# Kernel tuning notes

Hardware: AMD Instinct MI355X
Metric: run time of the kernel (lower is better)

The kernel has to match this reference:

```python
import jax, jax.numpy as jnp
import numpy as np

Z, Y, X = 16, 128, 128
B = 2
N_R, N_L = 12000, 20000   # active voxels per batch element (radar / lidar)
C = 64
IN_DIM = 4
NUM_LAYER = 2
K_LIST = (64, 32)         # knn fan-out = 64 / 2**layer
EPS = 1e-5


def _make_voxels(rng, n_per_batch):
    # unique voxel coords per batch, sorted by linear index (batch-major rows)
    out = []
    for b in range(B):
        lin = np.sort(rng.choice(Z * Y * X, size=n_per_batch, replace=False))
        z = lin // (Y * X); y = (lin // X) % Y; x = lin % X
        out.append(np.stack([np.full(n_per_batch, b), z, y, x], 1))
    return np.concatenate(out, 0).astype(np.int32)


def _nbr_map(coords):
    # 3x3x3 submanifold-conv rulebook: row index of each neighbor, -1 if absent
    b = coords[:, 0].astype(np.int64); z = coords[:, 1]; y = coords[:, 2]; x = coords[:, 3]
    keys = ((b * Z + z) * Y + y) * X + x  # globally sorted
    N = coords.shape[0]
    nbr = np.full((N, 27), -1, np.int64)
    k = 0
    for dz in (-1, 0, 1):
        for dy in (-1, 0, 1):
            for dx in (-1, 0, 1):
                nz, ny, nx = z + dz, y + dy, x + dx
                ok = (nz >= 0) & (nz < Z) & (ny >= 0) & (ny < Y) & (nx >= 0) & (nx < X)
                cand = ((b * Z + nz) * Y + ny) * X + nx
                pos = np.searchsorted(keys, cand)
                pos_c = np.clip(pos, 0, N - 1)
                hit = ok & (keys[pos_c] == cand)
                nbr[:, k] = np.where(hit, pos_c, -1)
                k += 1
    return nbr


def setup_inputs() -> dict:
    rng = np.random.default_rng(0)
    key = jax.random.key(0)
    ks = jax.random.split(key, 16)
    coordsR = _make_voxels(rng, N_R)
    coordsL = _make_voxels(rng, N_L)
    nbrR = _nbr_map(coordsR)
    nbrL = _nbr_map(coordsL)
    NLt = B * N_L
    # knn indices (global row ids into radar rows of same batch)
    knn0 = coordsL[:, 0:1].astype(np.int64) * N_R + rng.integers(0, N_R, (NLt, K_LIST[0]))
    knn1 = coordsL[:, 0:1].astype(np.int64) * N_R + rng.integers(0, N_R, (NLt, K_LIST[1]))
    sc = 1.0 / np.sqrt(27 * C).astype(np.float32)
    inp = {
        "featR": jax.random.normal(ks[0], (B * N_R, IN_DIM), jnp.float32),
        "featL": jax.random.normal(ks[1], (NLt, IN_DIM), jnp.float32),
        "img": jax.random.normal(ks[2], (B, 512), jnp.float32),
        "Win": jax.random.normal(ks[3], (2, IN_DIM, C), jnp.float32) * 0.1,
        "bin_": jnp.zeros((2, C), jnp.float32),
        # [layer, branch(R/L), conv(sp,subm_a,subm_b), 27, Cin, Cout]
        "Wconv": jax.random.normal(ks[4], (NUM_LAYER, 2, 3, 27, C, C), jnp.float32) * sc,
        "bconv": jnp.zeros((NUM_LAYER, 2, 3, C), jnp.float32),
        "bng": jnp.ones((NUM_LAYER, 2, 3, C), jnp.float32),
        "bnb": jnp.zeros((NUM_LAYER, 2, 3, C), jnp.float32),
        "Wimg": jax.random.normal(ks[5], (NUM_LAYER, 512, C), jnp.float32) * 0.05,
        "bimg": jnp.zeros((NUM_LAYER, C), jnp.float32),
        "Wval": jax.random.normal(ks[6], (NUM_LAYER, C, C), jnp.float32) * 0.125,
        "bval": jnp.zeros((NUM_LAYER, C), jnp.float32),
        "Wgate": jax.random.normal(ks[7], (NUM_LAYER, 2 * C, C), jnp.float32) * 0.09,
        "bgate": jnp.zeros((NUM_LAYER, C), jnp.float32),
        "Wbev": jax.random.normal(ks[8], (NUM_LAYER, 2, C * Z, C, 3, 3), jnp.float32) * (1.0 / np.sqrt(C * Z * 9).astype(np.float32)),
        "bbev": jnp.zeros((NUM_LAYER, 2, C), jnp.float32),
        "bntg": jnp.ones((NUM_LAYER, 2, C), jnp.float32),
        "bntb": jnp.zeros((NUM_LAYER, 2, C), jnp.float32),
        "nbrR": jnp.asarray(nbrR),
        "nbrL": jnp.asarray(nbrL),
        "knn0": jnp.asarray(knn0),
        "knn1": jnp.asarray(knn1),
        "coordsR": jnp.asarray(coordsR),
        "coordsL": jnp.asarray(coordsL),
    }
    return inp


def _bn1d(f, g, b):
    m = f.mean(0)
    v = f.var(0)
    return (f - m) / jnp.sqrt(v + EPS) * g + b


def _sconv(f, nbr, W, bias):
    # gather-scatter sparse 3D conv: out[n] = sum_k W[k] @ f[nbr[n,k]]
    mask = (nbr >= 0)[..., None].astype(f.dtype)
    g = f[jnp.clip(nbr, 0)] * mask                 # [N, 27, C]
    return jnp.einsum('nkc,kcd->nd', g, W) + bias


def _branch_block(f, nbr, Wc, bc, g, bt):
    # spconv -> bn -> relu, subm_a -> bn -> relu, subm_b -> bn -> relu
    for j in range(3):
        f = jax.nn.relu(_bn1d(_sconv(f, nbr, Wc[j], bc[j]), g[j], bt[j]))
    return f


def _to_bev(f, coords, Wt, bt, gg, gb):
    dense = jnp.zeros((B, Z, Y, X, C), f.dtype).at[
        coords[:, 0], coords[:, 1], coords[:, 2], coords[:, 3]].add(f)
    x2 = dense.transpose(0, 4, 1, 2, 3).reshape(B, C * Z, Y, X)  # 'b c z y x -> b (c z) y x'
    # ConvTranspose2d(k=3, s=1, p=1) == conv with swapped-IO, spatially flipped kernel, pad 1
    Wk = jnp.transpose(Wt, (1, 0, 2, 3))[:, :, ::-1, ::-1]
    out = jax.lax.conv_general_dilated(x2, Wk, (1, 1), ((1, 1), (1, 1)),
                                       dimension_numbers=('NCHW', 'OIHW', 'NCHW'))
    out = out + bt[:, None, None]
    m = out.mean((0, 2, 3), keepdims=True)
    v = out.var((0, 2, 3), keepdims=True)
    out = (out - m) / jnp.sqrt(v + EPS) * gg[:, None, None] + gb[:, None, None]
    return jax.nn.relu(out)


def reference(featR, featL, img, Win, bin_, Wconv, bconv, bng, bnb, Wimg, bimg,
              Wval, bval, Wgate, bgate, Wbev, bbev, bntg, bntb,
              nbrR, nbrL, knn0, knn1, coordsR, coordsL):
    fR = featR @ Win[0] + bin_[0]   # input_convR (1x1x1)
    fL = featL @ Win[1] + bin_[1]   # input_convL (1x1x1)
    knns = (knn0, knn1)
    bidL = coordsL[:, 0]
    bevs = []
    for l in range(NUM_LAYER):
        fR = _branch_block(fR, nbrR, Wconv[l, 0], bconv[l, 0], bng[l, 0], bnb[l, 0])
        fL = _branch_block(fL, nbrL, Wconv[l, 1], bconv[l, 1], bng[l, 1], bnb[l, 1])
        # knn cross-attention fusion: lidar queries K nearest radar voxels
        key = fR[knns[l]]                                        # [NL, K, C]
        val = jnp.einsum('nkc,cd->nkd', key, Wval[l]) + bval[l]
        attn = jax.nn.softmax(jnp.einsum('nc,nkc->nk', fL, key), axis=-1)
        fused = jnp.einsum('nk,nkd->nd', attn, val)
        imgf = jax.nn.sigmoid(img @ Wimg[l] + bimg[l])           # [B, C] weather condition
        fused = fused * imgf[bidL]
        gate = jax.nn.sigmoid(jnp.concatenate([fL, fused], -1) @ Wgate[l] + bgate[l])
        fL = fL + gate * fused
        bevs.append(_to_bev(fR, coordsR, Wbev[l, 0], bbev[l, 0], bntg[l, 0], bntb[l, 0]))
        bevs.append(_to_bev(fL, coordsL, Wbev[l, 1], bbev[l, 1], bntg[l, 1], bntb[l, 1]))
    return jnp.concatenate(bevs, axis=1)  # [B, 4*C, Y, X]
```

## Files before the change

kernel.cpp:

```cpp
#include <hip/hip_runtime.h>
#include <math.h>

#define NRT 24000
#define NLT 40000

static __device__ __forceinline__ float sigmoidf_(float x){ return 1.0f/(1.0f+expf(-x)); }

static __device__ __forceinline__ int xcd_swz(int bid, int nwg){
  int q = nwg>>3, r = nwg&7, x = bid&7, i = bid>>3;
  return (x<r ? x*(q+1) : r*(q+1)+(x-r)*q) + i;
}

__global__ void k_proj(const float* __restrict__ feat, const float* __restrict__ W,
                       const float* __restrict__ bias, float* __restrict__ out, int N){
  int i = blockIdx.x*256 + threadIdx.x;
  if (i >= N*64) return;
  int n = i >> 6, c = i & 63;
  const float* f = feat + n*4;
  out[i] = fmaf(f[0], W[c], fmaf(f[1], W[64+c], fmaf(f[2], W[128+c], fmaf(f[3], W[192+c], bias[c]))));
}

__global__ void k_mask(const int* __restrict__ nbr, int N, int* __restrict__ mask){
  int n = blockIdx.x*256+threadIdx.x;
  if (n>=N) return;
  const int* row = nbr + (size_t)n*27;
  int m=0;
  #pragma unroll
  for (int k=0;k<27;k++) if (row[k]>=0) m |= 1<<k;
  mask[n]=m;
}

__global__ void k_wsum(const int* __restrict__ mask, int N, int* __restrict__ wsum){
  int n = blockIdx.x*256+threadIdx.x;
  int pc = (n<N)? __popc(mask[n]) : 0;
  #pragma unroll
  for (int s=32;s;s>>=1) pc += __shfl_down(pc, s, 64);
  if ((threadIdx.x&63)==0) wsum[(blockIdx.x*256+threadIdx.x)>>6] = pc;
}

__global__ void k_scan(const int* __restrict__ in, int M, int* __restrict__ out){
  __shared__ int buf[704];
  for (int i=threadIdx.x;i<M;i+=256) buf[i]=in[i];
  __syncthreads();
  if (threadIdx.x==0){ int s=0; for (int i=0;i<M;i++){ int v=buf[i]; buf[i]=s; s+=v; } buf[M]=s; }
  __syncthreads();
  for (int i=threadIdx.x;i<=M;i+=256) out[i]=buf[i];
}

__global__ void k_noff(const int* __restrict__ mask, const int* __restrict__ woff,
                       int N, int* __restrict__ noff){
  int n = blockIdx.x*256+threadIdx.x;
  if (n>=N) return;
  int lane = threadIdx.x&63;
  int pc = __popc(mask[n]);
  int pre = pc;
  #pragma unroll
  for (int s=1;s<64;s<<=1){ int v=__shfl_up(pre, s, 64); if (lane>=s) pre+=v; }
  noff[n] = woff[n>>6] + pre - pc;
  if (n==N-1) noff[N] = woff[N>>6];
}

__global__ void k_kcnt2(const int* __restrict__ mask, int N, int* __restrict__ cnt2){
  int k = blockIdx.x>>3, seg = blockIdx.x&7;
  int s0 = seg*(N/8), s1 = s0 + N/8;
  int c=0;
  for (int n=s0+threadIdx.x;n<s1;n+=256) c += (mask[n]>>k)&1;
  __shared__ int ls[256];
  ls[threadIdx.x]=c; __syncthreads();
  for (int m=128;m;m>>=1){ if (threadIdx.x<m) ls[threadIdx.x]+=ls[threadIdx.x+m]; __syncthreads(); }
  if (threadIdx.x==0) cnt2[blockIdx.x]=ls[0];
}

__global__ void k_kfill2(const int* __restrict__ mask, int N, const int* __restrict__ off2,
                         unsigned* __restrict__ pairs){
  int w = (blockIdx.x*256+threadIdx.x)>>6;
  int lane = threadIdx.x&63;
  int k = w>>3, seg = w&7;
  int s0 = seg*(N/8), s1 = s0 + N/8;
  int base = off2[w];
  for (int n0=s0;n0<s1;n0+=64){
    int n = n0+lane;
    int v = (n<s1) && ((mask[n]>>k)&1);
    unsigned long long bal = __ballot(v);
    if (v) pairs[base + (int)__popcll(bal & ((1ull<<lane)-1))] = ((unsigned)k<<16)|(unsigned)n;
    base += (int)__popcll(bal);
  }
}

__global__ void k_wc(const float* __restrict__ Wconv, float* __restrict__ WcT){
  int i = blockIdx.x*256+threadIdx.x;
  if (i >= 12*27*16*64*4) return;
  int j = i & 3; int r = i >> 2;
  int d = r & 63; r >>= 6;
  int c4 = r & 15; r >>= 4;
  int k = r % 27; int lc = r / 27;
  WcT[i] = Wconv[(size_t)lc*110592 + (size_t)k*4096 + (size_t)(4*c4+j)*64 + d];
}

__global__ void k_spmm(const float* __restrict__ fin, const int* __restrict__ nbr,
                       const int* __restrict__ mask, const int* __restrict__ noff,
                       const int* __restrict__ off2, const unsigned* __restrict__ pairs,
                       const float* __restrict__ W, float* __restrict__ contrib, int nwaves){
  int wid = (blockIdx.x*256+threadIdx.x)>>6;
  int t = threadIdx.x&63;
  int total = off2[216];
  int a = (int)(((long long)wid*total)/nwaves);
  int b = (int)(((long long)(wid+1)*total)/nwaves);
  int kcur = -1;
  float4 wreg[16];
  for (int i=a;i<b;i++){
    unsigned pk = pairs[i];
    int k = pk>>16, n = pk&0xFFFF;
    if (k!=kcur){
      kcur=k;
      const float4* w4 = reinterpret_cast<const float4*>(W) + k*1024 + t;
      #pragma unroll
      for (int c4=0;c4<16;c4++) wreg[c4]=w4[c4*64];
    }
    int nb = nbr[(size_t)n*27+k];
    const float4* fr = reinterpret_cast<const float4*>(fin + (size_t)nb*64);
    float4 a4 = make_float4(0.f,0.f,0.f,0.f);
    #pragma unroll
    for (int c4=0;c4<16;c4++){
      float4 fv = fr[c4];
      a4.x = fmaf(fv.x, wreg[c4].x, a4.x);
      a4.y = fmaf(fv.y, wreg[c4].y, a4.y);
      a4.z = fmaf(fv.z, wreg[c4].z, a4.z);
      a4.w = fmaf(fv.w, wreg[c4].w, a4.w);
    }
    int rank = __popc(mask[n] & ((1<<k)-1));
    contrib[((size_t)noff[n]+rank)*64 + t] = (a4.x+a4.y)+(a4.z+a4.w);
  }
}

__global__ void k_sred(const float* __restrict__ contrib, const int* __restrict__ noff,
                       float* __restrict__ out, int N){
  int n = (blockIdx.x*256+threadIdx.x)>>6;
  if (n>=N) return;
  int t = threadIdx.x&63;
  int j0=noff[n], j1=noff[n+1];
  float s=0.f;
  for (int j=j0;j<j1;j++) s += contrib[(size_t)j*64+t];
  out[(size_t)n*64+t]=s;
}

__global__ void k_colsum(const float* __restrict__ f, int N, float* __restrict__ partial){
  int d = threadIdx.x & 63, sub = threadIdx.x >> 6;
  float s=0.f, s2=0.f;
  for (int n = blockIdx.x*4 + sub; n < N; n += 1024){
    float v = f[(size_t)n*64+d];
    s += v; s2 = fmaf(v,v,s2);
  }
  __shared__ float ls[4][64], ls2[4][64];
  ls[sub][d]=s; ls2[sub][d]=s2;
  __syncthreads();
  if (sub==0){
    s  = ls[0][d]+ls[1][d]+ls[2][d]+ls[3][d];
    s2 = ls2[0][d]+ls2[1][d]+ls2[2][d]+ls2[3][d];
    partial[(blockIdx.x*64+d)*2+0]=s;
    partial[(blockIdx.x*64+d)*2+1]=s2;
  }
}

__global__ void k_bnfin(const float* __restrict__ partial, int nblk, float invN,
                        const float* __restrict__ g, const float* __restrict__ b,
                        float* __restrict__ mv){
  int t = threadIdx.x, d = t & 63, sub = t >> 6;
  float s=0.f, s2=0.f;
  for (int i=sub;i<nblk;i+=4){ s += partial[(i*64+d)*2]; s2 += partial[(i*64+d)*2+1]; }
  __shared__ float ls[4][64], ls2[4][64];
  ls[sub][d]=s; ls2[sub][d]=s2;
  __syncthreads();
  if (sub==0){
    s  = ls[0][d]+ls[1][d]+ls[2][d]+ls[3][d];
    s2 = ls2[0][d]+ls2[1][d]+ls2[2][d]+ls2[3][d];
    float mean = s*invN;
    float var  = s2*invN - mean*mean;
    float rstd = 1.0f/sqrtf(var + 1e-5f);
    float sc = g[d]*rstd;
    mv[d*2]   = sc;
    mv[d*2+1] = b[d] - mean*sc;
  }
}

__global__ void k_bnrelu(const float* __restrict__ cv, const float* __restrict__ mv,
                         float* __restrict__ fout, int total){
  int i = blockIdx.x*256+threadIdx.x;
  if (i>=total) return;
  int c = i & 63;
  float v = fmaf(cv[i], mv[c*2], mv[c*2+1]);
  fout[i] = v>0.f? v:0.f;
}

__global__ void k_imgf(const float* __restrict__ img, const float* __restrict__ Wimg,
                       const float* __restrict__ bimg, float* __restrict__ imgf){
  int t = threadIdx.x;
  int b = t>>6, c = t&63;
  float s = bimg[c];
  const float* ir = img + b*512;
  for (int j=0;j<512;j++) s = fmaf(ir[j], Wimg[j*64+c], s);
  imgf[b*64+c] = sigmoidf_(s);
}

__global__ void k_attn(float* __restrict__ fL, const float* __restrict__ fR,
                       const int* __restrict__ knn, const int* __restrict__ coordsL,
                       const float* __restrict__ Wval, const float* __restrict__ bval,
                       const float* __restrict__ Wgate, const float* __restrict__ bgate,
                       const float* __restrict__ imgf, int K){
  __shared__ float keys[64*65];
  __shared__ float fls[64];
  __shared__ float aw[64];
  __shared__ float wks[64];
  __shared__ float fus[64];
  int n = blockIdx.x, t = threadIdx.x;
  float fl = fL[(size_t)n*64+t];
  fls[t] = fl;
  const int* kn = knn + (size_t)n*K;
  for (int k=0;k<K;k++){
    int r = kn[k];
    keys[k*65+t] = fR[(size_t)r*64+t];
  }
  __syncthreads();
  float s = -1e30f;
  if (t < K){
    const float* kr = keys + t*65;
    float a0 = 0.f;
    #pragma unroll
    for (int c=0;c<64;c++) a0 = fmaf(fls[c], kr[c], a0);
    s = a0;
  }
  float mx = s;
  #pragma unroll
  for (int m=32;m;m>>=1) mx = fmaxf(mx, __shfl_xor(mx, m, 64));
  float e = (t<K) ? expf(s-mx) : 0.f;
  float se = e;
  #pragma unroll
  for (int m=32;m;m>>=1) se += __shfl_xor(se, m, 64);
  aw[t] = e/se;
  __syncthreads();
  float wk = 0.f;
  for (int k=0;k<K;k++) wk = fmaf(aw[k], keys[k*65+t], wk);
  wks[t] = wk;
  __syncthreads();
  float fu = bval[t];
  #pragma unroll
  for (int c=0;c<64;c++) fu = fmaf(wks[c], Wval[c*64+t], fu);
  int bid = coordsL[n*4];
  fu *= imgf[bid*64+t];
  fus[t] = fu;
  __syncthreads();
  float gs = bgate[t];
  #pragma unroll
  for (int c=0;c<64;c++) gs = fmaf(fls[c], Wgate[c*64+t], gs);
  #pragma unroll
  for (int c=0;c<64;c++) gs = fmaf(fus[c], Wgate[(64+c)*64+t], gs);
  float gate = sigmoidf_(gs);
  fL[(size_t)n*64+t] = fl + gate*fu;
}

__global__ void k_grid(const int* __restrict__ coords, int N, int* __restrict__ grid){
  int n = blockIdx.x*256+threadIdx.x;
  if (n>=N) return;
  int b=coords[n*4], z=coords[n*4+1], y=coords[n*4+2], x=coords[n*4+3];
  grid[((b*128+y)*128+x)*16+z] = n;
}

__global__ void k_colbuild(const int* __restrict__ grid, int* __restrict__ ccnt,
                           int* __restrict__ cent){
  int col = blockIdx.x*256+threadIdx.x;
  if (col >= 2*128*128) return;
  const int* g = grid + col*16;
  int c=0;
  for (int z=0;z<16;z++){ int v=g[z]; if (v>=0) cent[col*16 + (c++)] = (v<<4)|z; }
  ccnt[col]=c;
}

__global__ void k_zbound(const int* __restrict__ coords, int N, int* __restrict__ zs){
  int n = blockIdx.x*256+threadIdx.x;
  if (n>=N) return;
  int key = coords[n*4]*16 + coords[n*4+1];
  int pk = (n>0) ? coords[(n-1)*4]*16 + coords[(n-1)*4+1] : -1;
  for (int kk=pk+1; kk<=key; kk++) zs[kk] = n;
  if (n==N-1){ for (int kk=key+1; kk<=32; kk++) zs[kk] = N; }
}

__global__ void k_wt3(const float* __restrict__ Wbev, float* __restrict__ Wt3){
  int i = blockIdx.x*256+threadIdx.x;
  if (i >= 4*9*16*16*64*4) return;
  int j = i & 3; int r = i >> 2;
  int o = r & 63; r >>= 6;
  int c4 = r & 15; r >>= 4;
  int z = r & 15; r >>= 4;
  int q = r % 9; int ls = r / 9;
  int c = 4*c4 + j;
  int ky = 2-q/3, kx = 2-q%3;
  Wt3[i] = Wbev[(size_t)ls*589824 + (size_t)(c*16+z)*576 + o*9 + ky*3 + kx];
}

__global__ void k_bevg(const float* __restrict__ f, const int* __restrict__ zs,
                       const float* __restrict__ Wt,
                       float* __restrict__ tmp, int CH){
  int blk = xcd_swz(blockIdx.x, gridDim.x);
  int task = blk / CH, chunk = blk % CH;
  int q = task % 9, z = task / 9;
  int t = threadIdx.x;
  const float4* w4 = reinterpret_cast<const float4*>(Wt + (size_t)(((q<<4)+z)<<12)) + t;
  float4 wreg[16];
  #pragma unroll
  for (int c4=0;c4<16;c4++) wreg[c4] = w4[c4*64];
  int s0 = zs[z], c0 = zs[z+1]-s0;
  int s1 = zs[16+z], c1 = zs[17+z]-s1;
  int total = c0 + c1;
  for (int i=chunk; i<total; i+=CH){
    int v = (i<c0) ? s0+i : s1+(i-c0);
    const float4* fr = reinterpret_cast<const float4*>(f + (size_t)v*64);
    float4 a = make_float4(0.f,0.f,0.f,0.f);
    #pragma unroll
    for (int c4=0;c4<16;c4++){
      float4 fv = fr[c4];
      a.x = fmaf(fv.x, wreg[c4].x, a.x);
      a.y = fmaf(fv.y, wreg[c4].y, a.y);
      a.z = fmaf(fv.z, wreg[c4].z, a.z);
      a.w = fmaf(fv.w, wreg[c4].w, a.w);
    }
    tmp[((size_t)v*9+q)*64 + t] = (a.x+a.y)+(a.z+a.w);
  }
}

__global__ void k_bevs(const float* __restrict__ tmp, const int* __restrict__ ccnt,
                       const int* __restrict__ cent, float* __restrict__ outp){
  int blk = xcd_swz(blockIdx.x, gridDim.x);
  int b = blk>>12; int rem = blk&4095; int y = rem>>5; int x0 = (rem&31)<<2;
  int t = threadIdx.x;
  float acc[4] = {0.f,0.f,0.f,0.f};
  #pragma unroll
  for (int dy=-1;dy<=1;dy++){
    int y2 = y+dy;
    if ((unsigned)y2 >= 128u) continue;
    int qb = (dy+1)*3 + 1;
    for (int cx=x0-1; cx<=x0+4; cx++){
      if ((unsigned)cx >= 128u) continue;
      int col = ((b<<7)+y2)*128 + cx;
      int cn = ccnt[col];
      const int* ce = cent + col*16;
      int d0 = cx - x0;
      for (int i=0;i<cn;i++){
        int rid = ce[i]>>4;
        const float* tb = tmp + (size_t)rid*576 + qb*64 + t;
        #pragma unroll
        for (int v=0;v<4;v++){
          int dx = d0 - v;
          if (dx>=-1 && dx<=1) acc[v] += tb[dx*64];
        }
      }
    }
  }
  float4 o4 = make_float4(acc[0],acc[1],acc[2],acc[3]);
  *reinterpret_cast<float4*>(outp + (size_t)b*(256*16384) + (size_t)t*16384 + y*128 + x0) = o4;
}

__global__ void k_bevstat(const float* __restrict__ outp, const float* __restrict__ g,
                          const float* __restrict__ b, float* __restrict__ mv){
  int ch = blockIdx.x, t = threadIdx.x;
  float s=0.f, s2=0.f;
  for (int bb=0;bb<2;bb++){
    const float* base = outp + (size_t)bb*(256*16384) + (size_t)ch*16384;
    for (int p=t;p<16384;p+=256){ float v = base[p]; s+=v; s2=fmaf(v,v,s2); }
  }
  __shared__ float ls[256], ls2[256];
  ls[t]=s; ls2[t]=s2; __syncthreads();
  for (int m=128;m;m>>=1){ if (t<m){ ls[t]+=ls[t+m]; ls2[t]+=ls2[t+m]; } __syncthreads(); }
  if (t==0){
    float mean = ls[0]*(1.0f/32768.0f);
    float var  = ls2[0]*(1.0f/32768.0f) - mean*mean;
    float rstd = 1.0f/sqrtf(var+1e-5f);
    float sc = g[ch]*rstd;
    mv[ch*2]=sc; mv[ch*2+1]=b[ch]-mean*sc;
  }
}

__global__ void k_bevbn(float* __restrict__ outp, const float* __restrict__ mv){
  int i = blockIdx.x*256+threadIdx.x;
  if (i >= 2*64*16384) return;
  int bb = i>>20; int r = i & ((1<<20)-1);
  int ch = r>>14; int p = r&16383;
  float* a = outp + (size_t)bb*(256*16384) + (size_t)ch*16384 + p;
  float v = fmaf(*a, mv[ch*2], mv[ch*2+1]);
  *a = v>0.f? v:0.f;
}

extern "C" void kernel_launch(void* const* d_in, const int* in_sizes, int n_in,
                              void* d_out, int out_size, void* d_ws, size_t ws_size,
                              hipStream_t stream){
  const float* featR = (const float*)d_in[0];
  const float* featL = (const float*)d_in[1];
  const float* img   = (const float*)d_in[2];
  const float* Win   = (const float*)d_in[3];
  const float* bin_  = (const float*)d_in[4];
  const float* Wconv = (const float*)d_in[5];
  const float* bng   = (const float*)d_in[7];
  const float* bnb   = (const float*)d_in[8];
  const float* Wimg  = (const float*)d_in[9];
  const float* bimg  = (const float*)d_in[10];
  const float* Wval  = (const float*)d_in[11];
  const float* bval  = (const float*)d_in[12];
  const float* Wgate = (const float*)d_in[13];
  const float* bgate = (const float*)d_in[14];
  const float* Wbev  = (const float*)d_in[15];
  const float* bntg  = (const float*)d_in[17];
  const float* bntb  = (const float*)d_in[18];
  const int* nbrR    = (const int*)d_in[19];
  const int* nbrL    = (const int*)d_in[20];
  const int* knn0    = (const int*)d_in[21];
  const int* knn1    = (const int*)d_in[22];
  const int* coordsR = (const int*)d_in[23];
  const int* coordsL = (const int*)d_in[24];
  float* outp = (float*)d_out;

  char* w = (char*)d_ws;
  auto alloc = [&](size_t bytes){ char* p = w; w += (bytes + 255) & ~(size_t)255; return p; };
  float* fRa = (float*)alloc((size_t)NRT*64*4);
  float* fLa = (float*)alloc((size_t)NLT*64*4);
  int*   gridR = (int*)alloc((size_t)2*128*128*16*4);
  int*   gridL = (int*)alloc((size_t)2*128*128*16*4);
  float* Wt3 = (float*)alloc((size_t)4*9*16*16*64*4*4);
  float* WcT = (float*)alloc((size_t)12*27*16*64*4*4);
  float* imgfbuf = (float*)alloc(2*64*4);
  float* partial = (float*)alloc((size_t)256*64*2*4);
  float* mv = (float*)alloc(64*2*4);
  int* ccntR = (int*)alloc((size_t)2*128*128*4);
  int* ccntL = (int*)alloc((size_t)2*128*128*4);
  int* centR = (int*)alloc((size_t)2*128*128*16*4);
  int* centL = (int*)alloc((size_t)2*128*128*16*4);
  int* zsR = (int*)alloc(33*4);
  int* zsL = (int*)alloc(33*4);
  int* maskR = (int*)alloc((size_t)NRT*4);
  int* maskL = (int*)alloc((size_t)NLT*4);
  int* wsumR = (int*)alloc(1024*4);
  int* wsumL = (int*)alloc(1024*4);
  int* woffR = (int*)alloc(1024*4);
  int* woffL = (int*)alloc(1024*4);
  int* noffR = (int*)alloc((size_t)(NRT+1)*4);
  int* noffL = (int*)alloc((size_t)(NLT+1)*4);
  int* cnt2R = (int*)alloc(256*4);
  int* cnt2L = (int*)alloc(256*4);
  int* off2R = (int*)alloc(256*4);
  int* off2L = (int*)alloc(256*4);
  unsigned* pairsR = (unsigned*)alloc((size_t)6*NRT*4);
  unsigned* pairsL = (unsigned*)alloc((size_t)6*NLT*4);
  char* big = alloc((size_t)NLT*576*4);
  float* cv      = (float*)big;
  float* contrib = (float*)(big + (size_t)16*1024*1024);
  float* tmp     = (float*)big;

  hipMemsetAsync(gridR, 0xFF, (size_t)2*128*128*16*4, stream);
  hipMemsetAsync(gridL, 0xFF, (size_t)2*128*128*16*4, stream);
  k_grid<<<(NRT+255)/256,256,0,stream>>>(coordsR, NRT, gridR);
  k_grid<<<(NLT+255)/256,256,0,stream>>>(coordsL, NLT, gridL);
  k_colbuild<<<(2*128*128+255)/256,256,0,stream>>>(gridR, ccntR, centR);
  k_colbuild<<<(2*128*128+255)/256,256,0,stream>>>(gridL, ccntL, centL);
  k_zbound<<<(NRT+255)/256,256,0,stream>>>(coordsR, NRT, zsR);
  k_zbound<<<(NLT+255)/256,256,0,stream>>>(coordsL, NLT, zsL);
  k_mask<<<(NRT+255)/256,256,0,stream>>>(nbrR, NRT, maskR);
  k_mask<<<(NLT+255)/256,256,0,stream>>>(nbrL, NLT, maskL);
  k_wsum<<<(NRT+255)/256,256,0,stream>>>(maskR, NRT, wsumR);
  k_wsum<<<(NLT+255)/256,256,0,stream>>>(maskL, NLT, wsumL);
  k_scan<<<1,256,0,stream>>>(wsumR, NRT/64, woffR);
  k_scan<<<1,256,0,stream>>>(wsumL, NLT/64, woffL);
  k_noff<<<(NRT+255)/256,256,0,stream>>>(maskR, woffR, NRT, noffR);
  k_noff<<<(NLT+255)/256,256,0,stream>>>(maskL, woffL, NLT, noffL);
  k_kcnt2<<<216,256,0,stream>>>(maskR, NRT, cnt2R);
  k_kcnt2<<<216,256,0,stream>>>(maskL, NLT, cnt2L);
  k_scan<<<1,256,0,stream>>>(cnt2R, 216, off2R);
  k_scan<<<1,256,0,stream>>>(cnt2L, 216, off2L);
  k_kfill2<<<54,256,0,stream>>>(maskR, NRT, off2R, pairsR);
  k_kfill2<<<54,256,0,stream>>>(maskL, NLT, off2L, pairsL);
  k_wt3<<<(4*9*16*16*64*4+255)/256,256,0,stream>>>(Wbev, Wt3);
  k_wc<<<(12*27*16*64*4+255)/256,256,0,stream>>>(Wconv, WcT);

  k_proj<<<(NRT*64+255)/256,256,0,stream>>>(featR, Win,     bin_,    fRa, NRT);
  k_proj<<<(NLT*64+255)/256,256,0,stream>>>(featL, Win+256, bin_+64, fLa, NLT);

  const int CH = 32;
  const int NWV = 2048;
  for (int l=0;l<2;l++){
    for (int j=0;j<3;j++){
      const float* Wc = WcT + (size_t)((l*2+0)*3+j)*110592;
      k_spmm<<<NWV/4,256,0,stream>>>(fRa, nbrR, maskR, noffR, off2R, pairsR, Wc, contrib, NWV);
      k_sred<<<(NRT+3)/4,256,0,stream>>>(contrib, noffR, cv, NRT);
      k_colsum<<<256,256,0,stream>>>(cv, NRT, partial);
      k_bnfin<<<1,256,0,stream>>>(partial, 256, 1.0f/NRT,
                                  bng + ((l*2+0)*3+j)*64, bnb + ((l*2+0)*3+j)*64, mv);
      k_bnrelu<<<(NRT*64+255)/256,256,0,stream>>>(cv, mv, fRa, NRT*64);
    }
    for (int j=0;j<3;j++){
      const float* Wc = WcT + (size_t)((l*2+1)*3+j)*110592;
      k_spmm<<<NWV/4,256,0,stream>>>(fLa, nbrL, maskL, noffL, off2L, pairsL, Wc, contrib, NWV);
      k_sred<<<(NLT+3)/4,256,0,stream>>>(contrib, noffL, cv, NLT);
      k_colsum<<<256,256,0,stream>>>(cv, NLT, partial);
      k_bnfin<<<1,256,0,stream>>>(partial, 256, 1.0f/NLT,
                                  bng + ((l*2+1)*3+j)*64, bnb + ((l*2+1)*3+j)*64, mv);
      k_bnrelu<<<(NLT*64+255)/256,256,0,stream>>>(cv, mv, fLa, NLT*64);
    }
    k_imgf<<<1,128,0,stream>>>(img, Wimg + (size_t)l*512*64, bimg + l*64, imgfbuf);
    const int* knn = (l==0)? knn0 : knn1;
    int K = (l==0)? 64 : 32;
    k_attn<<<NLT,64,0,stream>>>(fLa, fRa, knn, coordsL,
                                Wval + (size_t)l*4096, bval + l*64,
                                Wgate + (size_t)l*8192, bgate + l*64,
                                imgfbuf, K);
    {
      float* op = outp + (size_t)(2*l)*64*16384;
      const float* wt = Wt3 + (size_t)(l*2+0)*589824;
      k_bevg<<<144*CH,64,0,stream>>>(fRa, zsR, wt, tmp, CH);
      k_bevs<<<2*128*32,64,0,stream>>>(tmp, ccntR, centR, op);
      k_bevstat<<<64,256,0,stream>>>(op, bntg + (l*2+0)*64, bntb + (l*2+0)*64, mv);
      k_bevbn<<<(2*64*16384+255)/256,256,0,stream>>>(op, mv);
    }
    {
      float* op = outp + (size_t)(2*l+1)*64*16384;
      const float* wt = Wt3 + (size_t)(l*2+1)*589824;
      k_bevg<<<144*CH,64,0,stream>>>(fLa, zsL, wt, tmp, CH);
      k_bevs<<<2*128*32,64,0,stream>>>(tmp, ccntL, centL, op);
      k_bevstat<<<64,256,0,stream>>>(op, bntg + (l*2+1)*64, bntb + (l*2+1)*64, mv);
      k_bevbn<<<(2*64*16384+255)/256,256,0,stream>>>(op, mv);
    }
  }
}
```

Baseline: 3.442 ms.

## Fuse sparse reduce with BN column stats, add nontemporal hints, retune spmm/bev grids

The neighbor-contribution reduction (k_sred) now also accumulates per-channel sum and sum-of-squares, so the separate k_colsum pass that re-read the conv output is removed and the partial count rises to 1024 blocks. Contributions and BEV temporaries are written and read with nontemporal hints to avoid polluting caches with streaming data. The spmm wave count is raised and k_bevg uses four waves per block with fewer chunks. Together these aim to cut launches and global memory traffic, at the cost of more partials to finalize and possible cache-policy side effects.

```diff
diff --git a/kernel.cpp b/kernel.cpp
--- a/kernel.cpp
+++ b/kernel.cpp
@@ -129,36 +129,31 @@
       a4.w = fmaf(fv.w, wreg[c4].w, a4.w);
     }
     int rank = __popc(mask[n] & ((1<<k)-1));
-    contrib[((size_t)noff[n]+rank)*64 + t] = (a4.x+a4.y)+(a4.z+a4.w);
+    __builtin_nontemporal_store((a4.x+a4.y)+(a4.z+a4.w),
+                                &contrib[((size_t)noff[n]+rank)*64 + t]);
   }
 }
 
 __global__ void k_sred(const float* __restrict__ contrib, const int* __restrict__ noff,
-                       float* __restrict__ out, int N){
-  int n = (blockIdx.x*256+threadIdx.x)>>6;
-  if (n>=N) return;
-  int t = threadIdx.x&63;
-  int j0=noff[n], j1=noff[n+1];
-  float s=0.f;
-  for (int j=j0;j<j1;j++) s += contrib[(size_t)j*64+t];
-  out[(size_t)n*64+t]=s;
-}
-
-__global__ void k_colsum(const float* __restrict__ f, int N, float* __restrict__ partial){
-  int d = threadIdx.x & 63, sub = threadIdx.x >> 6;
+                       float* __restrict__ out, int N, float* __restrict__ partial){
+  int t = threadIdx.x & 63, wv = threadIdx.x >> 6;
+  int gw = blockIdx.x*4 + wv;
   float s=0.f, s2=0.f;
-  for (int n = blockIdx.x*4 + sub; n < N; n += 1024){
-    float v = f[(size_t)n*64+d];
+  for (int n=gw; n<N; n+=4096){
+    int j0=noff[n], j1=noff[n+1];
+    float v=0.f;
+    for (int j=j0;j<j1;j++) v += __builtin_nontemporal_load(&contrib[(size_t)j*64+t]);
+    out[(size_t)n*64+t]=v;
     s += v; s2 = fmaf(v,v,s2);
   }
   __shared__ float ls[4][64], ls2[4][64];
-  ls[sub][d]=s; ls2[sub][d]=s2;
-  __syncthreads();
-  if (sub==0){
-    s  = ls[0][d]+ls[1][d]+ls[2][d]+ls[3][d];
-    s2 = ls2[0][d]+ls2[1][d]+ls2[2][d]+ls2[3][d];
-    partial[(blockIdx.x*64+d)*2+0]=s;
-    partial[(blockIdx.x*64+d)*2+1]=s2;
+  ls[wv][t]=s; ls2[wv][t]=s2;
+  __syncthreads();
+  if (wv==0){
+    s  = ls[0][t]+ls[1][t]+ls[2][t]+ls[3][t];
+    s2 = ls2[0][t]+ls2[1][t]+ls2[2][t]+ls2[3][t];
+    partial[(blockIdx.x*64+t)*2+0]=s;
+    partial[(blockIdx.x*64+t)*2+1]=s2;
   }
 }
 
@@ -303,7 +298,7 @@
   int blk = xcd_swz(blockIdx.x, gridDim.x);
   int task = blk / CH, chunk = blk % CH;
   int q = task % 9, z = task / 9;
-  int t = threadIdx.x;
+  int t = threadIdx.x & 63, wv = threadIdx.x >> 6;
   const float4* w4 = reinterpret_cast<const float4*>(Wt + (size_t)(((q<<4)+z)<<12)) + t;
   float4 wreg[16];
   #pragma unroll
@@ -311,7 +306,7 @@
   int s0 = zs[z], c0 = zs[z+1]-s0;
   int s1 = zs[16+z], c1 = zs[17+z]-s1;
   int total = c0 + c1;
-  for (int i=chunk; i<total; i+=CH){
+  for (int i=chunk*4+wv; i<total; i+=CH*4){
     int v = (i<c0) ? s0+i : s1+(i-c0);
     const float4* fr = reinterpret_cast<const float4*>(f + (size_t)v*64);
     float4 a = make_float4(0.f,0.f,0.f,0.f);
@@ -323,7 +318,7 @@
       a.z = fmaf(fv.z, wreg[c4].z, a.z);
       a.w = fmaf(fv.w, wreg[c4].w, a.w);
     }
-    tmp[((size_t)v*9+q)*64 + t] = (a.x+a.y)+(a.z+a.w);
+    __builtin_nontemporal_store((a.x+a.y)+(a.z+a.w), &tmp[((size_t)v*9+q)*64 + t]);
   }
 }
 
@@ -350,7 +345,7 @@
         #pragma unroll
         for (int v=0;v<4;v++){
           int dx = d0 - v;
-          if (dx>=-1 && dx<=1) acc[v] += tb[dx*64];
+          if (dx>=-1 && dx<=1) acc[v] += __builtin_nontemporal_load(&tb[dx*64]);
         }
       }
     }
@@ -426,7 +421,7 @@
   float* Wt3 = (float*)alloc((size_t)4*9*16*16*64*4*4);
   float* WcT = (float*)alloc((size_t)12*27*16*64*4*4);
   float* imgfbuf = (float*)alloc(2*64*4);
-  float* partial = (float*)alloc((size_t)256*64*2*4);
+  float* partial = (float*)alloc((size_t)1024*64*2*4);
   float* mv = (float*)alloc(64*2*4);
   int* ccntR = (int*)alloc((size_t)2*128*128*4);
   int* ccntL = (int*)alloc((size_t)2*128*128*4);
@@ -481,24 +476,22 @@
   k_proj<<<(NRT*64+255)/256,256,0,stream>>>(featR, Win,     bin_,    fRa, NRT);
   k_proj<<<(NLT*64+255)/256,256,0,stream>>>(featL, Win+256, bin_+64, fLa, NLT);
 
-  const int CH = 32;
-  const int NWV = 2048;
+  const int CH = 8;
+  const int NWV = 8192;
   for (int l=0;l<2;l++){
     for (int j=0;j<3;j++){
       const float* Wc = WcT + (size_t)((l*2+0)*3+j)*110592;
       k_spmm<<<NWV/4,256,0,stream>>>(fRa, nbrR, maskR, noffR, off2R, pairsR, Wc, contrib, NWV);
-      k_sred<<<(NRT+3)/4,256,0,stream>>>(contrib, noffR, cv, NRT);
-      k_colsum<<<256,256,0,stream>>>(cv, NRT, partial);
-      k_bnfin<<<1,256,0,stream>>>(partial, 256, 1.0f/NRT,
+      k_sred<<<1024,256,0,stream>>>(contrib, noffR, cv, NRT, partial);
+      k_bnfin<<<1,256,0,stream>>>(partial, 1024, 1.0f/NRT,
                                   bng + ((l*2+0)*3+j)*64, bnb + ((l*2+0)*3+j)*64, mv);
       k_bnrelu<<<(NRT*64+255)/256,256,0,stream>>>(cv, mv, fRa, NRT*64);
     }
     for (int j=0;j<3;j++){
       const float* Wc = WcT + (size_t)((l*2+1)*3+j)*110592;
       k_spmm<<<NWV/4,256,0,stream>>>(fLa, nbrL, maskL, noffL, off2L, pairsL, Wc, contrib, NWV);
-      k_sred<<<(NLT+3)/4,256,0,stream>>>(contrib, noffL, cv, NLT);
-      k_colsum<<<256,256,0,stream>>>(cv, NLT, partial);
-      k_bnfin<<<1,256,0,stream>>>(partial, 256, 1.0f/NLT,
+      k_sred<<<1024,256,0,stream>>>(contrib, noffL, cv, NLT, partial);
+      k_bnfin<<<1,256,0,stream>>>(partial, 1024, 1.0f/NLT,
                                   bng + ((l*2+1)*3+j)*64, bnb + ((l*2+1)*3+j)*64, mv);
       k_bnrelu<<<(NLT*64+255)/256,256,0,stream>>>(cv, mv, fLa, NLT*64);
     }
@@ -512,7 +505,7 @@
     {
       float* op = outp + (size_t)(2*l)*64*16384;
       const float* wt = Wt3 + (size_t)(l*2+0)*589824;
-      k_bevg<<<144*CH,64,0,stream>>>(fRa, zsR, wt, tmp, CH);
+      k_bevg<<<144*CH,256,0,stream>>>(fRa, zsR, wt, tmp, CH);
       k_bevs<<<2*128*32,64,0,stream>>>(tmp, ccntR, centR, op);
       k_bevstat<<<64,256,0,stream>>>(op, bntg + (l*2+0)*64, bntb + (l*2+0)*64, mv);
       k_bevbn<<<(2*64*16384+255)/256,256,0,stream>>>(op, mv);
@@ -520,7 +513,7 @@
     {
       float* op = outp + (size_t)(2*l+1)*64*16384;
       const float* wt = Wt3 + (size_t)(l*2+1)*589824;
-      k_bevg<<<144*CH,64,0,stream>>>(fLa, zsL, wt, tmp, CH);
+      k_bevg<<<144*CH,256,0,stream>>>(fLa, zsL, wt, tmp, CH);
       k_bevs<<<2*128*32,64,0,stream>>>(tmp, ccntL, centL, op);
       k_bevstat<<<64,256,0,stream>>>(op, bntg + (l*2+1)*64, bntb + (l*2+1)*64, mv);
       k_bevbn<<<(2*64*16384+255)/256,256,0,stream>>>(op, mv);
```

Result: faster. 3.299 ms (-4.2%).
